# Performance work log

Hardware: AMD Instinct MI355X
Metric: run time of the kernel (lower is better)

## Reference

```python
import jax, jax.numpy as jnp
import numpy as np

H = 1024
B = 8192

def setup_inputs() -> dict:
    key = jax.random.key(0)
    ks = jax.random.split(key, 8)
    s = 1.0 / np.sqrt(H)
    return {
        "x": jax.random.normal(ks[0], (B, H), jnp.float32),
        "h": jax.random.normal(ks[1], (B, H), jnp.float32),
        "W_ih_w": jax.random.normal(ks[2], (3 * H, H), jnp.float32) * s,
        "W_ih_b": jax.random.normal(ks[3], (3 * H,), jnp.float32) * s,
        "U_r_w": jax.random.normal(ks[4], (H, H), jnp.float32) * s,
        "U_z_w": jax.random.normal(ks[5], (H, H), jnp.float32) * s,
        "U_n_w": jax.random.normal(ks[6], (H, H), jnp.float32) * s,
        "U_n_b": jax.random.normal(ks[7], (H,), jnp.float32) * s,
    }

def reference(x, h, W_ih_w, W_ih_b, U_r_w, U_z_w, U_n_w, U_n_b):
    # fused input projection: (B, 3H)
    x_proj = x @ W_ih_w.T + W_ih_b
    r_x, z_x, n_x = jnp.split(x_proj, 3, axis=-1)
    # per-gate hidden matmuls (transpose_U=False path)
    r_h = h @ U_r_w.T
    z_h = h @ U_z_w.T
    n_h = h @ U_n_w.T + U_n_b
    r = jax.nn.sigmoid(r_x + r_h)
    z = jax.nn.sigmoid(z_x + z_h)
    n = jnp.tanh(n_x + r * n_h)
    return (1.0 - z) * n + z * h
```

## Files before the change

kernel.cpp:

```cpp
#include <hip/hip_runtime.h>
#include <hip/hip_bf16.h>
#include <cstdint>

#define HDIM 1024
#define BM 128
#define BN 64
#define BKK 32
#define NT (HDIM / BKK)

typedef __attribute__((ext_vector_type(8))) __bf16 bf16x8;
typedef __attribute__((ext_vector_type(8))) unsigned short u16x8;
typedef __attribute__((ext_vector_type(4))) float f32x4;

static __device__ __forceinline__ unsigned short f2b(float f) {
    __hip_bfloat16 h = __float2bfloat16(f);
    return __builtin_bit_cast(unsigned short, h);
}

static __device__ __forceinline__ void barrier_fence() {
    asm volatile("" ::: "memory");
    __builtin_amdgcn_s_barrier();
    asm volatile("" ::: "memory");
}

__global__ void __launch_bounds__(256) cvt_all(
    const float* __restrict__ x, const float* __restrict__ h,
    const float* __restrict__ wih, const float* __restrict__ ur,
    const float* __restrict__ uz, const float* __restrict__ un,
    unsigned short* __restrict__ wb, unsigned short* __restrict__ urb,
    unsigned short* __restrict__ uzb, unsigned short* __restrict__ unb,
    unsigned short* __restrict__ xb, unsigned short* __restrict__ hb) {
    int b = blockIdx.x;
    const float* src; unsigned short* dst; int idx;
    if (b < 3072)       { src = wih; dst = wb;  idx = b; }
    else if (b < 4096)  { src = ur;  dst = urb; idx = b - 3072; }
    else if (b < 5120)  { src = uz;  dst = uzb; idx = b - 4096; }
    else if (b < 6144)  { src = un;  dst = unb; idx = b - 5120; }
    else if (b < 14336) { src = x;   dst = xb;  idx = b - 6144; }
    else                { src = h;   dst = hb;  idx = b - 14336; }
    int i = idx * 256 + threadIdx.x;
    float4 v = ((const float4*)src)[i];
    ushort4 o;
    o.x = f2b(v.x); o.y = f2b(v.y); o.z = f2b(v.z); o.w = f2b(v.w);
    ((ushort4*)dst)[i] = o;
}

template<bool XHB>
__global__ void __launch_bounds__(256, 2)
gru_fused(const float* __restrict__ hg,
          const unsigned short* __restrict__ xb, const unsigned short* __restrict__ hb,
          const float* __restrict__ xg32, const float* __restrict__ hg32,
          const unsigned short* __restrict__ wih,
          const unsigned short* __restrict__ ur,
          const unsigned short* __restrict__ uz,
          const unsigned short* __restrict__ un,
          const float* __restrict__ bih, const float* __restrict__ bun,
          float* __restrict__ out) {
    __shared__ __align__(16) unsigned short smem[2][20480];

    const int tid  = threadIdx.x;
    const int lane = tid & 63;
    const int wv   = tid >> 6;
    const int wm   = wv >> 1;
    const int wn   = wv & 1;
    const int lr   = lane & 15;
    const int ls   = lane >> 4;
    const int m0   = blockIdx.y * BM;
    const int n0   = blockIdx.x * BN;

    const unsigned short* wb6[6] = {
        wih + (size_t)n0 * HDIM,
        wih + (size_t)(HDIM + n0) * HDIM,
        wih + (size_t)(2 * HDIM + n0) * HDIM,
        ur  + (size_t)n0 * HDIM,
        uz  + (size_t)n0 * HDIM,
        un  + (size_t)n0 * HDIM
    };

    const int wr  = tid >> 2;
    const int wsl = (tid & 3) ^ ((tid >> 3) & 3);

    f32x4 acc[4][4][2];
#pragma unroll
    for (int g = 0; g < 4; ++g)
#pragma unroll
        for (int mf = 0; mf < 4; ++mf)
#pragma unroll
            for (int nf = 0; nf < 2; ++nf)
                acc[g][mf][nf] = f32x4{0.f, 0.f, 0.f, 0.f};

    auto STAGE = [&](int bufi, int kt) {
        const int k0 = kt * BKK;
        unsigned short* sb = &smem[bufi][0];
        float4 fx[2][2], fh[2][2];
        if constexpr (!XHB) {
#pragma unroll
            for (int half = 0; half < 2; ++half) {
                const int c2 = half * 256 + tid;
                const int r2 = c2 >> 2;
                const int sl = c2 & 3;
                const float* gx = xg32 + (size_t)(m0 + r2) * HDIM + k0 + sl * 8;
                const float* gh = hg32 + (size_t)(m0 + r2) * HDIM + k0 + sl * 8;
                fx[half][0] = ((const float4*)gx)[0];
                fx[half][1] = ((const float4*)gx)[1];
                fh[half][0] = ((const float4*)gh)[0];
                fh[half][1] = ((const float4*)gh)[1];
            }
        }
#pragma unroll
        for (int mi = 0; mi < 6; ++mi) {
            const unsigned short* g = wb6[mi] + (size_t)wr * HDIM + k0 + wsl * 8;
            __builtin_amdgcn_global_load_lds(
                (const __attribute__((address_space(1))) void*)g,
                (__attribute__((address_space(3))) void*)(sb + 8192 + mi * 2048 + wv * 512),
                16, 0, 0);
        }
        if constexpr (XHB) {
#pragma unroll
            for (int half = 0; half < 2; ++half) {
                const int c2 = half * 256 + tid;
                const int r2 = c2 >> 2;
                const int sl = (c2 & 3) ^ ((c2 >> 3) & 3);
                const unsigned short* gx = xb + (size_t)(m0 + r2) * HDIM + k0 + sl * 8;
                const unsigned short* gh = hb + (size_t)(m0 + r2) * HDIM + k0 + sl * 8;
                __builtin_amdgcn_global_load_lds(
                    (const __attribute__((address_space(1))) void*)gx,
                    (__attribute__((address_space(3))) void*)(sb + half * 2048 + wv * 512),
                    16, 0, 0);
                __builtin_amdgcn_global_load_lds(
                    (const __attribute__((address_space(1))) void*)gh,
                    (__attribute__((address_space(3))) void*)(sb + 4096 + half * 2048 + wv * 512),
                    16, 0, 0);
            }
        } else {
#pragma unroll
            for (int half = 0; half < 2; ++half) {
                const int c2 = half * 256 + tid;
                const int r2 = c2 >> 2;
                const int sp = (c2 & 3) ^ ((c2 >> 3) & 3);
                u16x8 px, ph;
#pragma unroll
                for (int q = 0; q < 4; ++q) {
                    px[q]     = f2b(fx[half][0][q]);
                    px[q + 4] = f2b(fx[half][1][q]);
                    ph[q]     = f2b(fh[half][0][q]);
                    ph[q + 4] = f2b(fh[half][1][q]);
                }
                *(u16x8*)(sb + r2 * 32 + sp * 8)        = px;
                *(u16x8*)(sb + 4096 + r2 * 32 + sp * 8) = ph;
            }
        }
    };

    auto COMPUTE = [&](int bufi) {
        const unsigned short* sb = &smem[bufi][0];
        const int sel = (lr >> 1) & 3;
        const int fo  = (ls ^ sel) << 3;
        bf16x8 ax[4], ah[4];
#pragma unroll
        for (int mf = 0; mf < 4; ++mf) {
            const int row = wm * 64 + mf * 16 + lr;
            ax[mf] = *(const bf16x8*)(sb + row * 32 + fo);
            ah[mf] = *(const bf16x8*)(sb + 4096 + row * 32 + fo);
        }
#pragma unroll
        for (int mi = 0; mi < 6; ++mi) {
            const unsigned short* wt = sb + 8192 + mi * 2048;
            bf16x8 b0 = *(const bf16x8*)(wt + (wn * 32 + lr) * 32 + fo);
            bf16x8 b1 = *(const bf16x8*)(wt + (wn * 32 + 16 + lr) * 32 + fo);
            const int g = (mi == 0 || mi == 3) ? 0 : (mi == 1 || mi == 4) ? 1 : (mi == 2) ? 2 : 3;
            const bf16x8* a = (mi < 3) ? ax : ah;
#pragma unroll
            for (int mf = 0; mf < 4; ++mf) {
                acc[g][mf][0] = __builtin_amdgcn_mfma_f32_16x16x32_bf16(a[mf], b0, acc[g][mf][0], 0, 0, 0);
                acc[g][mf][1] = __builtin_amdgcn_mfma_f32_16x16x32_bf16(a[mf], b1, acc[g][mf][1], 0, 0, 0);
            }
        }
    };

    auto WAITN = [&]() {
        if constexpr (XHB) asm volatile("s_waitcnt vmcnt(10)" ::: "memory");
        else               asm volatile("s_waitcnt vmcnt(6) lgkmcnt(0)" ::: "memory");
    };

    STAGE(0, 0);
#pragma unroll 1
    for (int kt = 0; kt < NT - 2; kt += 2) {
        STAGE(1, kt + 1); WAITN(); barrier_fence();
        COMPUTE(0);       barrier_fence();
        STAGE(0, kt + 2); WAITN(); barrier_fence();
        COMPUTE(1);       barrier_fence();
    }
    STAGE(1, NT - 1); WAITN(); barrier_fence();
    COMPUTE(0);       barrier_fence();
    asm volatile("s_waitcnt vmcnt(0) lgkmcnt(0)" ::: "memory");
    __builtin_amdgcn_s_barrier();
    asm volatile("" ::: "memory");
    COMPUTE(1);

#pragma unroll
    for (int nf = 0; nf < 2; ++nf) {
        const int gc = n0 + wn * 32 + nf * 16 + lr;
        const float br  = bih[gc];
        const float bz  = bih[HDIM + gc];
        const float bnx = bih[2 * HDIM + gc];
        const float bn2 = bun[gc];
#pragma unroll
        for (int mf = 0; mf < 4; ++mf) {
            const f32x4 aR = acc[0][mf][nf];
            const f32x4 aZ = acc[1][mf][nf];
            const f32x4 aX = acc[2][mf][nf];
            const f32x4 aH = acc[3][mf][nf];
#pragma unroll
            for (int rr = 0; rr < 4; ++rr) {
                const int gr = m0 + wm * 64 + mf * 16 + ls * 4 + rr;
                const float rv = 1.f / (1.f + __expf(-(aR[rr] + br)));
                const float zv = 1.f / (1.f + __expf(-(aZ[rr] + bz)));
                const float nv = tanhf(aX[rr] + bnx + rv * (aH[rr] + bn2));
                const float hv = hg[(size_t)gr * HDIM + gc];
                out[(size_t)gr * HDIM + gc] = (1.f - zv) * nv + zv * hv;
            }
        }
    }
}

extern "C" void kernel_launch(void* const* d_in, const int* in_sizes, int n_in,
                              void* d_out, int out_size, void* d_ws, size_t ws_size,
                              hipStream_t stream) {
    const float* x   = (const float*)d_in[0];
    const float* h   = (const float*)d_in[1];
    const float* Wih = (const float*)d_in[2];
    const float* bih = (const float*)d_in[3];
    const float* Ur  = (const float*)d_in[4];
    const float* Uz  = (const float*)d_in[5];
    const float* Un  = (const float*)d_in[6];
    const float* bun = (const float*)d_in[7];
    float* out = (float*)d_out;

    unsigned short* wsp  = (unsigned short*)d_ws;
    unsigned short* wihb = wsp;
    unsigned short* urb  = wihb + 3 * 1024 * 1024;
    unsigned short* uzb  = urb + 1024 * 1024;
    unsigned short* unb  = uzb + 1024 * 1024;
    unsigned short* xb   = unb + 1024 * 1024;
    unsigned short* hb   = xb + 8 * 1024 * 1024;

    const bool xhb = ws_size >= 46137344ull;

    cvt_all<<<xhb ? 22528 : 6144, 256, 0, stream>>>(
        x, h, Wih, Ur, Uz, Un, wihb, urb, uzb, unb, xb, hb);

    dim3 grid(HDIM / BN, 8192 / BM);
    if (xhb)
        gru_fused<true><<<grid, 256, 0, stream>>>(
            h, xb, hb, nullptr, nullptr, wihb, urb, uzb, unb, bih, bun, out);
    else
        gru_fused<false><<<grid, 256, 0, stream>>>(
            h, nullptr, nullptr, x, h, wihb, urb, uzb, unb, bih, bun, out);
}
```

Measured before the change: 142.4 us.

## Rewrite main GRU GEMM with 256-row tiles, 8 waves and interleaved staging

The fast path now uses 512-thread blocks with 256-row M tiles and a 1D grid with a block-index swizzle that groups tiles for better L2 reuse of weights and activations. Each K step is split into four MFMA clusters, and the global-to-LDS loads for the next tile (W, then X, then H) are issued between them under s_setprio, so memory transfers overlap with matrix work. This trades occupancy and LDS (larger shared buffer, one vmcnt(0) wait per tile) for fewer weight reloads per output row and tighter overlap. The fp32 fallback kernel is kept separately, essentially unchanged.

Result: slower. 157.8 us (+10.8%).

```diff
diff --git a/kernel.cpp b/kernel.cpp
--- a/kernel.cpp
+++ b/kernel.cpp
@@ -3,7 +3,7 @@
 #include <cstdint>
 
 #define HDIM 1024
-#define BM 128
+#define BM 256
 #define BN 64
 #define BKK 32
 #define NT (HDIM / BKK)
@@ -45,18 +45,31 @@
     ((ushort4*)dst)[i] = o;
 }
 
-template<bool XHB>
-__global__ void __launch_bounds__(256, 2)
-gru_fused(const float* __restrict__ hg,
-          const unsigned short* __restrict__ xb, const unsigned short* __restrict__ hb,
-          const float* __restrict__ xg32, const float* __restrict__ hg32,
-          const unsigned short* __restrict__ wih,
-          const unsigned short* __restrict__ ur,
-          const unsigned short* __restrict__ uz,
-          const unsigned short* __restrict__ un,
-          const float* __restrict__ bih, const float* __restrict__ bun,
-          float* __restrict__ out) {
-    __shared__ __align__(16) unsigned short smem[2][20480];
+template<int MH, int NF>
+__device__ __forceinline__ void mm_cluster(f32x4 (&acc)[4][4][2],
+        const bf16x8 (&ax)[4], const bf16x8 (&ah)[4], const bf16x8 (&bq)[6]) {
+#pragma unroll
+    for (int mi = 0; mi < 6; ++mi) {
+        const int g = (mi == 0 || mi == 3) ? 0 : (mi == 1 || mi == 4) ? 1 : (mi == 2) ? 2 : 3;
+#pragma unroll
+        for (int m2 = 0; m2 < 2; ++m2) {
+            const int mf = MH * 2 + m2;
+            acc[g][mf][NF] = __builtin_amdgcn_mfma_f32_16x16x32_bf16(
+                (mi < 3) ? ax[mf] : ah[mf], bq[mi], acc[g][mf][NF], 0, 0, 0);
+        }
+    }
+}
+
+__global__ void __launch_bounds__(512, 2)
+gru_fused8(const float* __restrict__ hg,
+           const unsigned short* __restrict__ xb, const unsigned short* __restrict__ hb,
+           const unsigned short* __restrict__ wih,
+           const unsigned short* __restrict__ ur,
+           const unsigned short* __restrict__ uz,
+           const unsigned short* __restrict__ un,
+           const float* __restrict__ bih, const float* __restrict__ bun,
+           float* __restrict__ out) {
+    __shared__ __align__(16) unsigned short smem[2][28672];
 
     const int tid  = threadIdx.x;
     const int lane = tid & 63;
@@ -65,8 +78,13 @@
     const int wn   = wv & 1;
     const int lr   = lane & 15;
     const int ls   = lane >> 4;
-    const int m0   = blockIdx.y * BM;
-    const int n0   = blockIdx.x * BN;
+    const int sel  = (lr >> 1) & 3;
+    const int fo   = (ls ^ sel) << 3;
+
+    const int bid = blockIdx.x;
+    const int swz = (bid & 7) * 64 + (bid >> 3);
+    const int m0  = (swz & 31) * BM;
+    const int n0  = (swz >> 5) * BN;
 
     const unsigned short* wb6[6] = {
         wih + (size_t)n0 * HDIM,
@@ -77,6 +95,183 @@
         un  + (size_t)n0 * HDIM
     };
 
+    f32x4 acc[4][4][2];
+#pragma unroll
+    for (int g = 0; g < 4; ++g)
+#pragma unroll
+        for (int mf = 0; mf < 4; ++mf)
+#pragma unroll
+            for (int nf = 0; nf < 2; ++nf)
+                acc[g][mf][nf] = f32x4{0.f, 0.f, 0.f, 0.f};
+
+    auto STAGE_W = [&](unsigned short* nb, int kt) {
+        const int k0 = kt * BKK;
+#pragma unroll
+        for (int l = 0; l < 3; ++l) {
+            const int id = l * 512 + tid;
+            const int mi = id >> 8;
+            const int c  = id & 255;
+            const int r  = c >> 2;
+            const int sl = (c & 3) ^ ((c >> 3) & 3);
+            const unsigned short* g = wb6[mi] + (size_t)r * HDIM + k0 + sl * 8;
+            __builtin_amdgcn_global_load_lds(
+                (const __attribute__((address_space(1))) void*)g,
+                (__attribute__((address_space(3))) void*)(nb + 16384 + l * 4096 + wv * 512),
+                16, 0, 0);
+        }
+    };
+    auto STAGE_X = [&](unsigned short* nb, int kt) {
+        const int k0 = kt * BKK;
+#pragma unroll
+        for (int half = 0; half < 2; ++half) {
+            const int c  = half * 512 + tid;
+            const int r  = c >> 2;
+            const int sl = (c & 3) ^ ((c >> 3) & 3);
+            const unsigned short* g = xb + (size_t)(m0 + r) * HDIM + k0 + sl * 8;
+            __builtin_amdgcn_global_load_lds(
+                (const __attribute__((address_space(1))) void*)g,
+                (__attribute__((address_space(3))) void*)(nb + half * 4096 + wv * 512),
+                16, 0, 0);
+        }
+    };
+    auto STAGE_H = [&](unsigned short* nb, int kt) {
+        const int k0 = kt * BKK;
+#pragma unroll
+        for (int half = 0; half < 2; ++half) {
+            const int c  = half * 512 + tid;
+            const int r  = c >> 2;
+            const int sl = (c & 3) ^ ((c >> 3) & 3);
+            const unsigned short* g = hb + (size_t)(m0 + r) * HDIM + k0 + sl * 8;
+            __builtin_amdgcn_global_load_lds(
+                (const __attribute__((address_space(1))) void*)g,
+                (__attribute__((address_space(3))) void*)(nb + 8192 + half * 4096 + wv * 512),
+                16, 0, 0);
+        }
+    };
+
+    auto TILE = [&](int cur, int ktn, bool stage) {
+        const unsigned short* sb = &smem[cur][0];
+        unsigned short* nb = &smem[cur ^ 1][0];
+        bf16x8 ax[4], ah[4], bq[6];
+
+        {
+            const int ra0 = (wm * 64 + 0 * 16 + lr) * 32 + fo;
+            const int ra1 = (wm * 64 + 1 * 16 + lr) * 32 + fo;
+            ax[0] = *(const bf16x8*)(sb + ra0);
+            ah[0] = *(const bf16x8*)(sb + 8192 + ra0);
+            ax[1] = *(const bf16x8*)(sb + ra1);
+            ah[1] = *(const bf16x8*)(sb + 8192 + ra1);
+            const int rb = (wn * 32 + 0 * 16 + lr) * 32 + fo;
+#pragma unroll
+            for (int mi = 0; mi < 6; ++mi)
+                bq[mi] = *(const bf16x8*)(sb + 16384 + mi * 2048 + rb);
+        }
+        if (stage) STAGE_W(nb, ktn);
+        barrier_fence();
+        asm volatile("s_waitcnt lgkmcnt(0)" ::: "memory");
+        __builtin_amdgcn_sched_barrier(0);
+        __builtin_amdgcn_s_setprio(1);
+        mm_cluster<0, 0>(acc, ax, ah, bq);
+        __builtin_amdgcn_s_setprio(0);
+        barrier_fence();
+
+        {
+            const int ra2 = (wm * 64 + 2 * 16 + lr) * 32 + fo;
+            const int ra3 = (wm * 64 + 3 * 16 + lr) * 32 + fo;
+            ax[2] = *(const bf16x8*)(sb + ra2);
+            ah[2] = *(const bf16x8*)(sb + 8192 + ra2);
+            ax[3] = *(const bf16x8*)(sb + ra3);
+            ah[3] = *(const bf16x8*)(sb + 8192 + ra3);
+        }
+        if (stage) STAGE_X(nb, ktn);
+        barrier_fence();
+        asm volatile("s_waitcnt lgkmcnt(0)" ::: "memory");
+        __builtin_amdgcn_sched_barrier(0);
+        __builtin_amdgcn_s_setprio(1);
+        mm_cluster<1, 0>(acc, ax, ah, bq);
+        __builtin_amdgcn_s_setprio(0);
+        barrier_fence();
+
+        {
+            const int rb = (wn * 32 + 1 * 16 + lr) * 32 + fo;
+#pragma unroll
+            for (int mi = 0; mi < 6; ++mi)
+                bq[mi] = *(const bf16x8*)(sb + 16384 + mi * 2048 + rb);
+        }
+        if (stage) STAGE_H(nb, ktn);
+        barrier_fence();
+        asm volatile("s_waitcnt lgkmcnt(0)" ::: "memory");
+        __builtin_amdgcn_sched_barrier(0);
+        __builtin_amdgcn_s_setprio(1);
+        mm_cluster<0, 1>(acc, ax, ah, bq);
+        __builtin_amdgcn_s_setprio(0);
+        barrier_fence();
+
+        __builtin_amdgcn_s_setprio(1);
+        mm_cluster<1, 1>(acc, ax, ah, bq);
+        __builtin_amdgcn_s_setprio(0);
+        asm volatile("s_waitcnt vmcnt(0)" ::: "memory");
+        barrier_fence();
+    };
+
+    STAGE_W(&smem[0][0], 0);
+    STAGE_X(&smem[0][0], 0);
+    STAGE_H(&smem[0][0], 0);
+    asm volatile("s_waitcnt vmcnt(0)" ::: "memory");
+    barrier_fence();
+
+#pragma unroll 1
+    for (int t = 0; t < NT - 1; ++t)
+        TILE(t & 1, t + 1, true);
+    TILE((NT - 1) & 1, 0, false);
+
+#pragma unroll
+    for (int nf = 0; nf < 2; ++nf) {
+        const int gc = n0 + wn * 32 + nf * 16 + lr;
+        const float br  = bih[gc];
+        const float bz  = bih[HDIM + gc];
+        const float bnx = bih[2 * HDIM + gc];
+        const float bn2 = bun[gc];
+#pragma unroll
+        for (int mf = 0; mf < 4; ++mf) {
+#pragma unroll
+            for (int rr = 0; rr < 4; ++rr) {
+                const int gr = m0 + wm * 64 + mf * 16 + ls * 4 + rr;
+                const float rv = 1.f / (1.f + __expf(-(acc[0][mf][nf][rr] + br)));
+                const float zv = 1.f / (1.f + __expf(-(acc[1][mf][nf][rr] + bz)));
+                const float nv = tanhf(acc[2][mf][nf][rr] + bnx + rv * (acc[3][mf][nf][rr] + bn2));
+                const float hv = hg[(size_t)gr * HDIM + gc];
+                out[(size_t)gr * HDIM + gc] = (1.f - zv) * nv + zv * hv;
+            }
+        }
+    }
+}
+
+__global__ void __launch_bounds__(256, 2)
+gru_fused_fb(const float* __restrict__ hg,
+             const float* __restrict__ xg32, const float* __restrict__ hg32,
+             const unsigned short* __restrict__ wih,
+             const unsigned short* __restrict__ ur,
+             const unsigned short* __restrict__ uz,
+             const unsigned short* __restrict__ un,
+             const float* __restrict__ bih, const float* __restrict__ bun,
+             float* __restrict__ out) {
+    __shared__ __align__(16) unsigned short smem[2][20480];
+    const int tid  = threadIdx.x;
+    const int lane = tid & 63;
+    const int wv   = tid >> 6;
+    const int wm   = wv >> 1;
+    const int wn   = wv & 1;
+    const int lr   = lane & 15;
+    const int ls   = lane >> 4;
+    const int m0   = blockIdx.y * 128;
+    const int n0   = blockIdx.x * BN;
+
+    const unsigned short* wb6[6] = {
+        wih + (size_t)n0 * HDIM, wih + (size_t)(HDIM + n0) * HDIM,
+        wih + (size_t)(2 * HDIM + n0) * HDIM, ur + (size_t)n0 * HDIM,
+        uz + (size_t)n0 * HDIM, un + (size_t)n0 * HDIM
+    };
     const int wr  = tid >> 2;
     const int wsl = (tid & 3) ^ ((tid >> 3) & 3);
 
@@ -93,19 +288,17 @@
         const int k0 = kt * BKK;
         unsigned short* sb = &smem[bufi][0];
         float4 fx[2][2], fh[2][2];
-        if constexpr (!XHB) {
-#pragma unroll
-            for (int half = 0; half < 2; ++half) {
-                const int c2 = half * 256 + tid;
-                const int r2 = c2 >> 2;
-                const int sl = c2 & 3;
-                const float* gx = xg32 + (size_t)(m0 + r2) * HDIM + k0 + sl * 8;
-                const float* gh = hg32 + (size_t)(m0 + r2) * HDIM + k0 + sl * 8;
-                fx[half][0] = ((const float4*)gx)[0];
-                fx[half][1] = ((const float4*)gx)[1];
-                fh[half][0] = ((const float4*)gh)[0];
-                fh[half][1] = ((const float4*)gh)[1];
-            }
+#pragma unroll
+        for (int half = 0; half < 2; ++half) {
+            const int c2 = half * 256 + tid;
+            const int r2 = c2 >> 2;
+            const int sl = c2 & 3;
+            const float* gx = xg32 + (size_t)(m0 + r2) * HDIM + k0 + sl * 8;
+            const float* gh = hg32 + (size_t)(m0 + r2) * HDIM + k0 + sl * 8;
+            fx[half][0] = ((const float4*)gx)[0];
+            fx[half][1] = ((const float4*)gx)[1];
+            fh[half][0] = ((const float4*)gh)[0];
+            fh[half][1] = ((const float4*)gh)[1];
         }
 #pragma unroll
         for (int mi = 0; mi < 6; ++mi) {
@@ -115,43 +308,23 @@
                 (__attribute__((address_space(3))) void*)(sb + 8192 + mi * 2048 + wv * 512),
                 16, 0, 0);
         }
-        if constexpr (XHB) {
-#pragma unroll
-            for (int half = 0; half < 2; ++half) {
-                const int c2 = half * 256 + tid;
-                const int r2 = c2 >> 2;
-                const int sl = (c2 & 3) ^ ((c2 >> 3) & 3);
-                const unsigned short* gx = xb + (size_t)(m0 + r2) * HDIM + k0 + sl * 8;
-                const unsigned short* gh = hb + (size_t)(m0 + r2) * HDIM + k0 + sl * 8;
-                __builtin_amdgcn_global_load_lds(
-                    (const __attribute__((address_space(1))) void*)gx,
-                    (__attribute__((address_space(3))) void*)(sb + half * 2048 + wv * 512),
-                    16, 0, 0);
-                __builtin_amdgcn_global_load_lds(
-                    (const __attribute__((address_space(1))) void*)gh,
-                    (__attribute__((address_space(3))) void*)(sb + 4096 + half * 2048 + wv * 512),
-                    16, 0, 0);
+#pragma unroll
+        for (int half = 0; half < 2; ++half) {
+            const int c2 = half * 256 + tid;
+            const int r2 = c2 >> 2;
+            const int sp = (c2 & 3) ^ ((c2 >> 3) & 3);
+            u16x8 px, ph;
+#pragma unroll
+            for (int q = 0; q < 4; ++q) {
+                px[q]     = f2b(fx[half][0][q]);
+                px[q + 4] = f2b(fx[half][1][q]);
+                ph[q]     = f2b(fh[half][0][q]);
+                ph[q + 4] = f2b(fh[half][1][q]);
             }
-        } else {
-#pragma unroll
-            for (int half = 0; half < 2; ++half) {
-                const int c2 = half * 256 + tid;
-                const int r2 = c2 >> 2;
-                const int sp = (c2 & 3) ^ ((c2 >> 3) & 3);
-                u16x8 px, ph;
-#pragma unroll
-                for (int q = 0; q < 4; ++q) {
-                    px[q]     = f2b(fx[half][0][q]);
-                    px[q + 4] = f2b(fx[half][1][q]);
-                    ph[q]     = f2b(fh[half][0][q]);
-                    ph[q + 4] = f2b(fh[half][1][q]);
-                }
-                *(u16x8*)(sb + r2 * 32 + sp * 8)        = px;
-                *(u16x8*)(sb + 4096 + r2 * 32 + sp * 8) = ph;
-            }
-        }
-    };
-
+            *(u16x8*)(sb + r2 * 32 + sp * 8)        = px;
+            *(u16x8*)(sb + 4096 + r2 * 32 + sp * 8) = ph;
+        }
+    };
     auto COMPUTE = [&](int bufi) {
         const unsigned short* sb = &smem[bufi][0];
         const int sel = (lr >> 1) & 3;
@@ -177,11 +350,7 @@
             }
         }
     };
-
-    auto WAITN = [&]() {
-        if constexpr (XHB) asm volatile("s_waitcnt vmcnt(10)" ::: "memory");
-        else               asm volatile("s_waitcnt vmcnt(6) lgkmcnt(0)" ::: "memory");
-    };
+    auto WAITN = [&]() { asm volatile("s_waitcnt vmcnt(6) lgkmcnt(0)" ::: "memory"); };
 
     STAGE(0, 0);
 #pragma unroll 1
@@ -207,16 +376,12 @@
         const float bn2 = bun[gc];
 #pragma unroll
         for (int mf = 0; mf < 4; ++mf) {
-            const f32x4 aR = acc[0][mf][nf];
-            const f32x4 aZ = acc[1][mf][nf];
-            const f32x4 aX = acc[2][mf][nf];
-            const f32x4 aH = acc[3][mf][nf];
 #pragma unroll
             for (int rr = 0; rr < 4; ++rr) {
                 const int gr = m0 + wm * 64 + mf * 16 + ls * 4 + rr;
-                const float rv = 1.f / (1.f + __expf(-(aR[rr] + br)));
-                const float zv = 1.f / (1.f + __expf(-(aZ[rr] + bz)));
-                const float nv = tanhf(aX[rr] + bnx + rv * (aH[rr] + bn2));
+                const float rv = 1.f / (1.f + __expf(-(acc[0][mf][nf][rr] + br)));
+                const float zv = 1.f / (1.f + __expf(-(acc[1][mf][nf][rr] + bz)));
+                const float nv = tanhf(acc[2][mf][nf][rr] + bnx + rv * (acc[3][mf][nf][rr] + bn2));
                 const float hv = hg[(size_t)gr * HDIM + gc];
                 out[(size_t)gr * HDIM + gc] = (1.f - zv) * nv + zv * hv;
             }
@@ -250,11 +415,12 @@
     cvt_all<<<xhb ? 22528 : 6144, 256, 0, stream>>>(
         x, h, Wih, Ur, Uz, Un, wihb, urb, uzb, unb, xb, hb);
 
-    dim3 grid(HDIM / BN, 8192 / BM);
-    if (xhb)
-        gru_fused<true><<<grid, 256, 0, stream>>>(
-            h, xb, hb, nullptr, nullptr, wihb, urb, uzb, unb, bih, bun, out);
-    else
-        gru_fused<false><<<grid, 256, 0, stream>>>(
-            h, nullptr, nullptr, x, h, wihb, urb, uzb, unb, bih, bun, out);
-}
+    if (xhb) {
+        gru_fused8<<<512, 512, 0, stream>>>(
+            h, xb, hb, wihb, urb, uzb, unb, bih, bun, out);
+    } else {
+        dim3 grid(HDIM / BN, 8192 / 128);
+        gru_fused_fb<<<grid, 256, 0, stream>>>(
+            h, x, h, wihb, urb, uzb, unb, bih, bun, out);
+    }
+}
```

## Use 32x32x16 MFMA tiles with swizzled block order in GRU kernel

Applied to the files above, without the earlier changes.

The bf16-input path now uses a dedicated kernel built on 32x32x16 MFMA instructions instead of 16x16x32. Each wave holds fewer accumulator tiles and issues fewer LDS fragment reads per MFMA. The kernel also remaps a 1D grid with an XCD-style block swizzle to improve L2 reuse of weights and activations, and precomputes incrementing global pointers. The fp32 fallback path is kept as a separate kernel. The epilogue row mapping changes to the 32x32 accumulator layout, which could introduce indexing errors.

New measurement: 157.1 us. 1.1x slower.

```diff
diff --git a/kernel.cpp b/kernel.cpp
--- a/kernel.cpp
+++ b/kernel.cpp
@@ -3,14 +3,12 @@
 #include <cstdint>
 
 #define HDIM 1024
-#define BM 128
-#define BN 64
-#define BKK 32
-#define NT (HDIM / BKK)
+#define NT 32
 
 typedef __attribute__((ext_vector_type(8))) __bf16 bf16x8;
 typedef __attribute__((ext_vector_type(8))) unsigned short u16x8;
 typedef __attribute__((ext_vector_type(4))) float f32x4;
+typedef __attribute__((ext_vector_type(16))) float f32x16;
 
 static __device__ __forceinline__ unsigned short f2b(float f) {
     __hip_bfloat16 h = __float2bfloat16(f);
@@ -45,19 +43,163 @@
     ((ushort4*)dst)[i] = o;
 }
 
-template<bool XHB>
 __global__ void __launch_bounds__(256, 2)
-gru_fused(const float* __restrict__ hg,
-          const unsigned short* __restrict__ xb, const unsigned short* __restrict__ hb,
-          const float* __restrict__ xg32, const float* __restrict__ hg32,
-          const unsigned short* __restrict__ wih,
-          const unsigned short* __restrict__ ur,
-          const unsigned short* __restrict__ uz,
-          const unsigned short* __restrict__ un,
-          const float* __restrict__ bih, const float* __restrict__ bun,
-          float* __restrict__ out) {
+gru32(const float* __restrict__ hg,
+      const unsigned short* __restrict__ xb, const unsigned short* __restrict__ hb,
+      const unsigned short* __restrict__ wih,
+      const unsigned short* __restrict__ ur,
+      const unsigned short* __restrict__ uz,
+      const unsigned short* __restrict__ un,
+      const float* __restrict__ bih, const float* __restrict__ bun,
+      float* __restrict__ out) {
     __shared__ __align__(16) unsigned short smem[2][20480];
 
+    const int tid  = threadIdx.x;
+    const int lane = tid & 63;
+    const int wv   = tid >> 6;
+    const int wm   = wv >> 1;
+    const int wn   = wv & 1;
+    const int l31  = lane & 31;
+    const int lh   = lane >> 5;
+
+    const int bid = blockIdx.x;
+    const int swz = (bid & 7) * 128 + (bid >> 3);
+    const int m0  = (swz & 63) * 128;
+    const int n0  = (swz >> 6) * 64;
+
+    const int wr  = tid >> 2;
+    const int wsl = (tid & 3) ^ ((tid >> 3) & 3);
+    const unsigned short* pw[6];
+    pw[0] = wih + (size_t)(n0 + wr) * HDIM + wsl * 8;
+    pw[1] = wih + (size_t)(HDIM + n0 + wr) * HDIM + wsl * 8;
+    pw[2] = wih + (size_t)(2 * HDIM + n0 + wr) * HDIM + wsl * 8;
+    pw[3] = ur  + (size_t)(n0 + wr) * HDIM + wsl * 8;
+    pw[4] = uz  + (size_t)(n0 + wr) * HDIM + wsl * 8;
+    pw[5] = un  + (size_t)(n0 + wr) * HDIM + wsl * 8;
+    const unsigned short* pxh[4];
+#pragma unroll
+    for (int half = 0; half < 2; ++half) {
+        const int c  = half * 256 + tid;
+        const int r  = c >> 2;
+        const int sl = (c & 3) ^ ((c >> 3) & 3);
+        pxh[half]     = xb + (size_t)(m0 + r) * HDIM + sl * 8;
+        pxh[2 + half] = hb + (size_t)(m0 + r) * HDIM + sl * 8;
+    }
+
+    const int arow  = wm * 64 + l31;
+    const int asel  = (arow >> 1) & 3;
+    const int aoff0 = arow * 32 + ((0 + lh) ^ asel) * 8;
+    const int aoff1 = arow * 32 + ((2 + lh) ^ asel) * 8;
+    const int wrow  = wn * 32 + l31;
+    const int bsel  = (wrow >> 1) & 3;
+    const int boff0 = 8192 + wrow * 32 + ((0 + lh) ^ bsel) * 8;
+    const int boff1 = 8192 + wrow * 32 + ((2 + lh) ^ bsel) * 8;
+
+    f32x16 acc[4][2];
+#pragma unroll
+    for (int g = 0; g < 4; ++g)
+#pragma unroll
+        for (int mc = 0; mc < 2; ++mc)
+#pragma unroll
+            for (int v = 0; v < 16; ++v)
+                acc[g][mc][v] = 0.f;
+
+    auto STAGE = [&](int bufi) {
+        unsigned short* nb = &smem[bufi][0];
+#pragma unroll
+        for (int mi = 0; mi < 6; ++mi) {
+            __builtin_amdgcn_global_load_lds(
+                (const __attribute__((address_space(1))) void*)pw[mi],
+                (__attribute__((address_space(3))) void*)(nb + 8192 + mi * 2048 + wv * 512),
+                16, 0, 0);
+            pw[mi] += 32;
+        }
+#pragma unroll
+        for (int half = 0; half < 2; ++half) {
+            __builtin_amdgcn_global_load_lds(
+                (const __attribute__((address_space(1))) void*)pxh[half],
+                (__attribute__((address_space(3))) void*)(nb + half * 2048 + wv * 512),
+                16, 0, 0);
+            pxh[half] += 32;
+            __builtin_amdgcn_global_load_lds(
+                (const __attribute__((address_space(1))) void*)pxh[2 + half],
+                (__attribute__((address_space(3))) void*)(nb + 4096 + half * 2048 + wv * 512),
+                16, 0, 0);
+            pxh[2 + half] += 32;
+        }
+    };
+
+    auto COMPUTE = [&](int bufi) {
+        const unsigned short* sb = &smem[bufi][0];
+        bf16x8 ax[2][2], ah[2][2];
+#pragma unroll
+        for (int mc = 0; mc < 2; ++mc) {
+            ax[mc][0] = *(const bf16x8*)(sb + aoff0 + mc * 1024);
+            ax[mc][1] = *(const bf16x8*)(sb + aoff1 + mc * 1024);
+            ah[mc][0] = *(const bf16x8*)(sb + 4096 + aoff0 + mc * 1024);
+            ah[mc][1] = *(const bf16x8*)(sb + 4096 + aoff1 + mc * 1024);
+        }
+#pragma unroll
+        for (int mi = 0; mi < 6; ++mi) {
+            bf16x8 b0 = *(const bf16x8*)(sb + boff0 + mi * 2048);
+            bf16x8 b1 = *(const bf16x8*)(sb + boff1 + mi * 2048);
+            const int g = (mi == 0 || mi == 3) ? 0 : (mi == 1 || mi == 4) ? 1 : (mi == 2) ? 2 : 3;
+#pragma unroll
+            for (int mc = 0; mc < 2; ++mc) {
+                acc[g][mc] = __builtin_amdgcn_mfma_f32_32x32x16_bf16(
+                    (mi < 3) ? ax[mc][0] : ah[mc][0], b0, acc[g][mc], 0, 0, 0);
+                acc[g][mc] = __builtin_amdgcn_mfma_f32_32x32x16_bf16(
+                    (mi < 3) ? ax[mc][1] : ah[mc][1], b1, acc[g][mc], 0, 0, 0);
+            }
+        }
+    };
+
+    auto WAITN = [&]() { asm volatile("s_waitcnt vmcnt(10)" ::: "memory"); };
+
+    STAGE(0);
+#pragma unroll 1
+    for (int kt = 0; kt < NT - 2; kt += 2) {
+        STAGE(1); WAITN(); barrier_fence();
+        COMPUTE(0); barrier_fence();
+        STAGE(0); WAITN(); barrier_fence();
+        COMPUTE(1); barrier_fence();
+    }
+    STAGE(1); WAITN(); barrier_fence();
+    COMPUTE(0); barrier_fence();
+    asm volatile("s_waitcnt vmcnt(0) lgkmcnt(0)" ::: "memory");
+    __builtin_amdgcn_s_barrier();
+    asm volatile("" ::: "memory");
+    COMPUTE(1);
+
+    const int gc = n0 + wn * 32 + l31;
+    const float br  = bih[gc];
+    const float bz  = bih[HDIM + gc];
+    const float bnx = bih[2 * HDIM + gc];
+    const float bn2 = bun[gc];
+#pragma unroll
+    for (int mc = 0; mc < 2; ++mc) {
+#pragma unroll
+        for (int v = 0; v < 16; ++v) {
+            const int gr = m0 + wm * 64 + mc * 32 + (v & 3) + 8 * (v >> 2) + 4 * lh;
+            const float rv = 1.f / (1.f + __expf(-(acc[0][mc][v] + br)));
+            const float zv = 1.f / (1.f + __expf(-(acc[1][mc][v] + bz)));
+            const float nv = tanhf(acc[2][mc][v] + bnx + rv * (acc[3][mc][v] + bn2));
+            const float hv = hg[(size_t)gr * HDIM + gc];
+            out[(size_t)gr * HDIM + gc] = (1.f - zv) * nv + zv * hv;
+        }
+    }
+}
+
+__global__ void __launch_bounds__(256, 2)
+gru_fused_fb(const float* __restrict__ hg,
+             const float* __restrict__ xg32, const float* __restrict__ hg32,
+             const unsigned short* __restrict__ wih,
+             const unsigned short* __restrict__ ur,
+             const unsigned short* __restrict__ uz,
+             const unsigned short* __restrict__ un,
+             const float* __restrict__ bih, const float* __restrict__ bun,
+             float* __restrict__ out) {
+    __shared__ __align__(16) unsigned short smem[2][20480];
     const int tid  = threadIdx.x;
     const int lane = tid & 63;
     const int wv   = tid >> 6;
@@ -65,18 +207,14 @@
     const int wn   = wv & 1;
     const int lr   = lane & 15;
     const int ls   = lane >> 4;
-    const int m0   = blockIdx.y * BM;
-    const int n0   = blockIdx.x * BN;
+    const int m0   = blockIdx.y * 128;
+    const int n0   = blockIdx.x * 64;
 
     const unsigned short* wb6[6] = {
-        wih + (size_t)n0 * HDIM,
-        wih + (size_t)(HDIM + n0) * HDIM,
-        wih + (size_t)(2 * HDIM + n0) * HDIM,
-        ur  + (size_t)n0 * HDIM,
-        uz  + (size_t)n0 * HDIM,
-        un  + (size_t)n0 * HDIM
-    };
-
+        wih + (size_t)n0 * HDIM, wih + (size_t)(HDIM + n0) * HDIM,
+        wih + (size_t)(2 * HDIM + n0) * HDIM, ur + (size_t)n0 * HDIM,
+        uz + (size_t)n0 * HDIM, un + (size_t)n0 * HDIM
+    };
     const int wr  = tid >> 2;
     const int wsl = (tid & 3) ^ ((tid >> 3) & 3);
 
@@ -90,22 +228,20 @@
                 acc[g][mf][nf] = f32x4{0.f, 0.f, 0.f, 0.f};
 
     auto STAGE = [&](int bufi, int kt) {
-        const int k0 = kt * BKK;
+        const int k0 = kt * 32;
         unsigned short* sb = &smem[bufi][0];
         float4 fx[2][2], fh[2][2];
-        if constexpr (!XHB) {
-#pragma unroll
-            for (int half = 0; half < 2; ++half) {
-                const int c2 = half * 256 + tid;
-                const int r2 = c2 >> 2;
-                const int sl = c2 & 3;
-                const float* gx = xg32 + (size_t)(m0 + r2) * HDIM + k0 + sl * 8;
-                const float* gh = hg32 + (size_t)(m0 + r2) * HDIM + k0 + sl * 8;
-                fx[half][0] = ((const float4*)gx)[0];
-                fx[half][1] = ((const float4*)gx)[1];
-                fh[half][0] = ((const float4*)gh)[0];
-                fh[half][1] = ((const float4*)gh)[1];
-            }
+#pragma unroll
+        for (int half = 0; half < 2; ++half) {
+            const int c2 = half * 256 + tid;
+            const int r2 = c2 >> 2;
+            const int sl = c2 & 3;
+            const float* gx = xg32 + (size_t)(m0 + r2) * HDIM + k0 + sl * 8;
+            const float* gh = hg32 + (size_t)(m0 + r2) * HDIM + k0 + sl * 8;
+            fx[half][0] = ((const float4*)gx)[0];
+            fx[half][1] = ((const float4*)gx)[1];
+            fh[half][0] = ((const float4*)gh)[0];
+            fh[half][1] = ((const float4*)gh)[1];
         }
 #pragma unroll
         for (int mi = 0; mi < 6; ++mi) {
@@ -115,43 +251,23 @@
                 (__attribute__((address_space(3))) void*)(sb + 8192 + mi * 2048 + wv * 512),
                 16, 0, 0);
         }
-        if constexpr (XHB) {
-#pragma unroll
-            for (int half = 0; half < 2; ++half) {
-                const int c2 = half * 256 + tid;
-                const int r2 = c2 >> 2;
-                const int sl = (c2 & 3) ^ ((c2 >> 3) & 3);
-                const unsigned short* gx = xb + (size_t)(m0 + r2) * HDIM + k0 + sl * 8;
-                const unsigned short* gh = hb + (size_t)(m0 + r2) * HDIM + k0 + sl * 8;
-                __builtin_amdgcn_global_load_lds(
-                    (const __attribute__((address_space(1))) void*)gx,
-                    (__attribute__((address_space(3))) void*)(sb + half * 2048 + wv * 512),
-                    16, 0, 0);
-                __builtin_amdgcn_global_load_lds(
-                    (const __attribute__((address_space(1))) void*)gh,
-                    (__attribute__((address_space(3))) void*)(sb + 4096 + half * 2048 + wv * 512),
-                    16, 0, 0);
+#pragma unroll
+        for (int half = 0; half < 2; ++half) {
+            const int c2 = half * 256 + tid;
+            const int r2 = c2 >> 2;
+            const int sp = (c2 & 3) ^ ((c2 >> 3) & 3);
+            u16x8 px, ph;
+#pragma unroll
+            for (int q = 0; q < 4; ++q) {
+                px[q]     = f2b(fx[half][0][q]);
+                px[q + 4] = f2b(fx[half][1][q]);
+                ph[q]     = f2b(fh[half][0][q]);
+                ph[q + 4] = f2b(fh[half][1][q]);
             }
-        } else {
-#pragma unroll
-            for (int half = 0; half < 2; ++half) {
-                const int c2 = half * 256 + tid;
-                const int r2 = c2 >> 2;
-                const int sp = (c2 & 3) ^ ((c2 >> 3) & 3);
-                u16x8 px, ph;
-#pragma unroll
-                for (int q = 0; q < 4; ++q) {
-                    px[q]     = f2b(fx[half][0][q]);
-                    px[q + 4] = f2b(fx[half][1][q]);
-                    ph[q]     = f2b(fh[half][0][q]);
-                    ph[q + 4] = f2b(fh[half][1][q]);
-                }
-                *(u16x8*)(sb + r2 * 32 + sp * 8)        = px;
-                *(u16x8*)(sb + 4096 + r2 * 32 + sp * 8) = ph;
-            }
-        }
-    };
-
+            *(u16x8*)(sb + r2 * 32 + sp * 8)        = px;
+            *(u16x8*)(sb + 4096 + r2 * 32 + sp * 8) = ph;
+        }
+    };
     auto COMPUTE = [&](int bufi) {
         const unsigned short* sb = &smem[bufi][0];
         const int sel = (lr >> 1) & 3;
@@ -177,11 +293,7 @@
             }
         }
     };
-
-    auto WAITN = [&]() {
-        if constexpr (XHB) asm volatile("s_waitcnt vmcnt(10)" ::: "memory");
-        else               asm volatile("s_waitcnt vmcnt(6) lgkmcnt(0)" ::: "memory");
-    };
+    auto WAITN = [&]() { asm volatile("s_waitcnt vmcnt(6) lgkmcnt(0)" ::: "memory"); };
 
     STAGE(0, 0);
 #pragma unroll 1
@@ -207,16 +319,12 @@
         const float bn2 = bun[gc];
 #pragma unroll
         for (int mf = 0; mf < 4; ++mf) {
-            const f32x4 aR = acc[0][mf][nf];
-            const f32x4 aZ = acc[1][mf][nf];
-            const f32x4 aX = acc[2][mf][nf];
-            const f32x4 aH = acc[3][mf][nf];
 #pragma unroll
             for (int rr = 0; rr < 4; ++rr) {
                 const int gr = m0 + wm * 64 + mf * 16 + ls * 4 + rr;
-                const float rv = 1.f / (1.f + __expf(-(aR[rr] + br)));
-                const float zv = 1.f / (1.f + __expf(-(aZ[rr] + bz)));
-                const float nv = tanhf(aX[rr] + bnx + rv * (aH[rr] + bn2));
+                const float rv = 1.f / (1.f + __expf(-(acc[0][mf][nf][rr] + br)));
+                const float zv = 1.f / (1.f + __expf(-(acc[1][mf][nf][rr] + bz)));
+                const float nv = tanhf(acc[2][mf][nf][rr] + bnx + rv * (acc[3][mf][nf][rr] + bn2));
                 const float hv = hg[(size_t)gr * HDIM + gc];
                 out[(size_t)gr * HDIM + gc] = (1.f - zv) * nv + zv * hv;
             }
@@ -250,11 +358,12 @@
     cvt_all<<<xhb ? 22528 : 6144, 256, 0, stream>>>(
         x, h, Wih, Ur, Uz, Un, wihb, urb, uzb, unb, xb, hb);
 
-    dim3 grid(HDIM / BN, 8192 / BM);
-    if (xhb)
-        gru_fused<true><<<grid, 256, 0, stream>>>(
-            h, xb, hb, nullptr, nullptr, wihb, urb, uzb, unb, bih, bun, out);
-    else
-        gru_fused<false><<<grid, 256, 0, stream>>>(
-            h, nullptr, nullptr, x, h, wihb, urb, uzb, unb, bih, bun, out);
-}
+    if (xhb) {
+        gru32<<<1024, 256, 0, stream>>>(
+            h, xb, hb, wihb, urb, uzb, unb, bih, bun, out);
+    } else {
+        dim3 grid(HDIM / 64, 8192 / 128);
+        gru_fused_fb<<<grid, 256, 0, stream>>>(
+            h, x, h, wihb, urb, uzb, unb, bih, bun, out);
+    }
+}
```
